# Performance work log

Measured on AMD Instinct MI355X. Metric: run time of the kernel, lower is better.

## Reference

```python
import jax, jax.numpy as jnp
import numpy as np

N, D = 262144, 512
EPS = 1e-6  # flax LayerNorm default


def setup_inputs() -> dict:
    key = jax.random.key(0)
    kx, kw = jax.random.split(key)
    x = jax.random.normal(kx, (N, D), dtype=jnp.float32)
    # LayerNorm params (flax defaults: scale init ones, bias init zeros)
    ln_scale = jnp.ones((D,), dtype=jnp.float32)
    ln_bias = jnp.zeros((D,), dtype=jnp.float32)
    # Dense params (lecun_normal kernel init approximated by scaled normal)
    kernel = jax.random.normal(kw, (D, D), dtype=jnp.float32) / jnp.sqrt(jnp.float32(D))
    bias = jnp.zeros((D,), dtype=jnp.float32)
    return {"x": x, "ln_scale": ln_scale, "ln_bias": ln_bias, "kernel": kernel, "bias": bias}


def reference(x, ln_scale, ln_bias, kernel, bias):
    # LayerNorm over last axis
    mu = jnp.mean(x, axis=-1, keepdims=True)
    var = jnp.mean(jnp.square(x - mu), axis=-1, keepdims=True)
    out = (x - mu) * jax.lax.rsqrt(var + EPS) * ln_scale + ln_bias
    # activation -> Dense -> residual add
    h = jax.nn.relu(out)
    return x + jnp.dot(h, kernel) + bias
```

## Files before the change

### kernel.cpp

```cpp
#include <hip/hip_runtime.h>
#include <hip/hip_bf16.h>

#define DD 512
#define BM 32
#define THREADS 512

typedef __attribute__((ext_vector_type(8))) short short8;
typedef __attribute__((ext_vector_type(4))) float f32x4;

__device__ __forceinline__ unsigned short f2bf(float f) {
  union { float f; unsigned u; } v; v.f = f;
  unsigned r = v.u + 0x7FFFu + ((v.u >> 16) & 1u);
  return (unsigned short)(r >> 16);
}
__device__ __forceinline__ float bf2f(unsigned short u) {
  union { unsigned u; float f; } v; v.u = ((unsigned)u) << 16;
  return v.f;
}

__global__ void prep_bpack(const float* __restrict__ W, unsigned short* __restrict__ Bpack) {
  const int tid = blockIdx.x * blockDim.x + threadIdx.x;
  const int n = tid & 511, k = tid >> 9;
  const float w = W[(size_t)k * DD + n];
  const int nb = n >> 4, lo = n & 15;
  const int kt = k >> 5, hi = (k >> 3) & 3, j = k & 7;
  const int lane = hi * 16 + lo;
  Bpack[(((size_t)(nb * 16 + kt)) * 64 + lane) * 8 + j] = f2bf(w);
}

__global__ __launch_bounds__(THREADS, 4)
void fused_ln_gemm(const float* __restrict__ x, const float* __restrict__ lns,
                   const float* __restrict__ lnb, const unsigned short* __restrict__ Bpack,
                   const float* __restrict__ bias, float* __restrict__ out) {
  __shared__ unsigned short Alds[BM * 512];
  __shared__ unsigned short Xlds[BM * 528];

  const int t = threadIdx.x;
  const long row0 = (long)blockIdx.x * BM;

  {
    const int r = t >> 4, g = t & 15;
    const float* xr = x + (row0 + r) * DD + g * 4;
    float4 v[8];
    float s = 0.f, s2 = 0.f;
    #pragma unroll
    for (int i = 0; i < 8; ++i) {
      v[i] = *(const float4*)(xr + i * 64);
      s  += (v[i].x + v[i].y) + (v[i].z + v[i].w);
      s2 += v[i].x * v[i].x + v[i].y * v[i].y + v[i].z * v[i].z + v[i].w * v[i].w;
    }
    #pragma unroll
    for (int m = 1; m < 16; m <<= 1) {
      s  += __shfl_xor(s,  m, 64);
      s2 += __shfl_xor(s2, m, 64);
    }
    const float mu   = s * (1.f / 512.f);
    const float var  = fmaxf(s2 * (1.f / 512.f) - mu * mu, 0.f);
    const float rstd = rsqrtf(var + 1e-6f);
    #pragma unroll
    for (int i = 0; i < 8; ++i) {
      const int c = g * 4 + i * 64;
      const float4 sc = *(const float4*)(lns + c);
      const float4 bi = *(const float4*)(lnb + c);
      float h0 = fmaxf((v[i].x - mu) * rstd * sc.x + bi.x, 0.f);
      float h1 = fmaxf((v[i].y - mu) * rstd * sc.y + bi.y, 0.f);
      float h2 = fmaxf((v[i].z - mu) * rstd * sc.z + bi.z, 0.f);
      float h3 = fmaxf((v[i].w - mu) * rstd * sc.w + bi.w, 0.f);
      ushort4 hu = { f2bf(h0), f2bf(h1), f2bf(h2), f2bf(h3) };
      ushort4 xu = { f2bf(v[i].x), f2bf(v[i].y), f2bf(v[i].z), f2bf(v[i].w) };
      unsigned a = (unsigned)(r * 1024 + g * 8 + i * 128) ^ (unsigned)((r & 7) << 4);
      *(ushort4*)((char*)Alds + a) = hu;
      *(ushort4*)(&Xlds[r * 528 + c]) = xu;
    }
  }
  __syncthreads();

  const int lane = t & 63, lo = lane & 15, hi = lane >> 4;
  const int wn = t >> 6;

  unsigned abase0, aswz0, abase1, aswz1;
  {
    const int r0 = lo;        abase0 = (unsigned)(r0 * 1024 + hi * 16); aswz0 = (unsigned)((r0 & 7) << 4);
    const int r1 = 16 + lo;   abase1 = (unsigned)(r1 * 1024 + hi * 16); aswz1 = (unsigned)((r1 & 7) << 4);
  }
  const short8* bbase = (const short8*)Bpack + (size_t)wn * 4096 + lane;

#define LOADB(dst, kt)                                                        \
  { dst##0 = bbase[(0 * 16 + (kt)) * 64];                                     \
    dst##1 = bbase[(1 * 16 + (kt)) * 64];                                     \
    dst##2 = bbase[(2 * 16 + (kt)) * 64];                                     \
    dst##3 = bbase[(3 * 16 + (kt)) * 64]; }

  short8 bA0, bA1, bA2, bA3, bB0, bB1, bB2, bB3, bC0, bC1, bC2, bC3;
  LOADB(bA, 0);
  LOADB(bB, 1);

  f32x4 acc00 = {}, acc01 = {}, acc02 = {}, acc03 = {};
  f32x4 acc10 = {}, acc11 = {}, acc12 = {}, acc13 = {};

  #pragma unroll
  for (int kt = 0; kt < 16; ++kt) {
    if (kt + 2 < 16) LOADB(bC, kt + 2);
    const short8 a0 = *(const short8*)((const char*)Alds + ((abase0 + (unsigned)kt * 64) ^ aswz0));
    const short8 a1 = *(const short8*)((const char*)Alds + ((abase1 + (unsigned)kt * 64) ^ aswz1));
    acc00 = __builtin_amdgcn_mfma_f32_16x16x32_bf16(a0, bA0, acc00, 0, 0, 0);
    acc10 = __builtin_amdgcn_mfma_f32_16x16x32_bf16(a1, bA0, acc10, 0, 0, 0);
    acc01 = __builtin_amdgcn_mfma_f32_16x16x32_bf16(a0, bA1, acc01, 0, 0, 0);
    acc11 = __builtin_amdgcn_mfma_f32_16x16x32_bf16(a1, bA1, acc11, 0, 0, 0);
    acc02 = __builtin_amdgcn_mfma_f32_16x16x32_bf16(a0, bA2, acc02, 0, 0, 0);
    acc12 = __builtin_amdgcn_mfma_f32_16x16x32_bf16(a1, bA2, acc12, 0, 0, 0);
    acc03 = __builtin_amdgcn_mfma_f32_16x16x32_bf16(a0, bA3, acc03, 0, 0, 0);
    acc13 = __builtin_amdgcn_mfma_f32_16x16x32_bf16(a1, bA3, acc13, 0, 0, 0);
    bA0 = bB0; bA1 = bB1; bA2 = bB2; bA3 = bB3;
    bB0 = bC0; bB1 = bC1; bB2 = bC2; bB3 = bC3;
  }
#undef LOADB

  f32x4 accs[2][4] = {{acc00, acc01, acc02, acc03}, {acc10, acc11, acc12, acc13}};
  #pragma unroll
  for (int m = 0; m < 2; ++m) {
    #pragma unroll
    for (int nt = 0; nt < 4; ++nt) {
      const int col = wn * 64 + nt * 16 + lo;
      const float bv = bias[col];
      #pragma unroll
      for (int q = 0; q < 4; ++q) {
        const int rloc = m * 16 + hi * 4 + q;
        const float xv = bf2f(Xlds[rloc * 528 + col]);
        out[(row0 + rloc) * DD + col] = xv + accs[m][nt][q] + bv;
      }
    }
  }
}

extern "C" void kernel_launch(void* const* d_in, const int* in_sizes, int n_in,
                              void* d_out, int out_size, void* d_ws, size_t ws_size,
                              hipStream_t stream) {
  const float* x    = (const float*)d_in[0];
  const float* lns  = (const float*)d_in[1];
  const float* lnb  = (const float*)d_in[2];
  const float* W    = (const float*)d_in[3];
  const float* bias = (const float*)d_in[4];
  float* out = (float*)d_out;
  unsigned short* Bpack = (unsigned short*)d_ws;

  const int nrows = in_sizes[0] / DD;

  prep_bpack<<<DD * DD / 256, 256, 0, stream>>>(W, Bpack);
  fused_ln_gemm<<<nrows / BM, THREADS, 0, stream>>>(x, lns, lnb, Bpack, bias, out);
}
```

Before: 336.7 us.

## Load x in MFMA output layout, keep residual in registers, drop Xlds buffer

Each thread now loads x elements at the positions its MFMA accumulators will write, keeping bf16-packed copies in registers for the residual instead of staging them in a 33KB LDS buffer. Row statistics are reduced via shuffles plus a small cross-wave LDS reduction, and the B-operand register prefetch pipeline is removed. Launch bounds are raised to 6 blocks per CU to exploit the lower LDS footprint. The trade-offs are strided 4-byte global loads instead of float4, scalar LDS stores for A, and loss of explicit B prefetching.

```diff
diff --git a/kernel.cpp b/kernel.cpp
--- a/kernel.cpp
+++ b/kernel.cpp
@@ -13,8 +13,8 @@
   unsigned r = v.u + 0x7FFFu + ((v.u >> 16) & 1u);
   return (unsigned short)(r >> 16);
 }
-__device__ __forceinline__ float bf2f(unsigned short u) {
-  union { unsigned u; float f; } v; v.u = ((unsigned)u) << 16;
+__device__ __forceinline__ float bf2f(unsigned u16) {
+  union { unsigned u; float f; } v; v.u = u16 << 16;
   return v.f;
 }
 
@@ -28,107 +28,144 @@
   Bpack[(((size_t)(nb * 16 + kt)) * 64 + lane) * 8 + j] = f2bf(w);
 }
 
-__global__ __launch_bounds__(THREADS, 4)
+__global__ __launch_bounds__(THREADS, 6)
 void fused_ln_gemm(const float* __restrict__ x, const float* __restrict__ lns,
                    const float* __restrict__ lnb, const unsigned short* __restrict__ Bpack,
                    const float* __restrict__ bias, float* __restrict__ out) {
   __shared__ unsigned short Alds[BM * 512];
-  __shared__ unsigned short Xlds[BM * 528];
+  __shared__ float s_lds[BM][8];
+  __shared__ float q_lds[BM][8];
 
   const int t = threadIdx.x;
+  const int lane = t & 63, lo = lane & 15, hi = lane >> 4;
+  const int wn = t >> 6;
   const long row0 = (long)blockIdx.x * BM;
 
+  float ps[8], pq[8];
+  unsigned xpk[16];
   {
-    const int r = t >> 4, g = t & 15;
-    const float* xr = x + (row0 + r) * DD + g * 4;
-    float4 v[8];
-    float s = 0.f, s2 = 0.f;
+    unsigned short tmp[4];
     #pragma unroll
-    for (int i = 0; i < 8; ++i) {
-      v[i] = *(const float4*)(xr + i * 64);
-      s  += (v[i].x + v[i].y) + (v[i].z + v[i].w);
-      s2 += v[i].x * v[i].x + v[i].y * v[i].y + v[i].z * v[i].z + v[i].w * v[i].w;
+    for (int m = 0; m < 2; ++m) {
+      #pragma unroll
+      for (int q = 0; q < 4; ++q) {
+        const float* xr = x + (row0 + m * 16 + hi * 4 + q) * DD + wn * 64 + lo;
+        const float v0 = xr[0], v1 = xr[16], v2 = xr[32], v3 = xr[48];
+        ps[m * 4 + q] = (v0 + v1) + (v2 + v3);
+        pq[m * 4 + q] = v0 * v0 + v1 * v1 + v2 * v2 + v3 * v3;
+        const unsigned short b0 = f2bf(v0), b1 = f2bf(v1), b2 = f2bf(v2), b3 = f2bf(v3);
+        if ((q & 1) == 0) {
+          tmp[0] = b0; tmp[1] = b1; tmp[2] = b2; tmp[3] = b3;
+        } else {
+          xpk[(m * 4 + 0) * 2 + (q >> 1)] = (unsigned)tmp[0] | ((unsigned)b0 << 16);
+          xpk[(m * 4 + 1) * 2 + (q >> 1)] = (unsigned)tmp[1] | ((unsigned)b1 << 16);
+          xpk[(m * 4 + 2) * 2 + (q >> 1)] = (unsigned)tmp[2] | ((unsigned)b2 << 16);
+          xpk[(m * 4 + 3) * 2 + (q >> 1)] = (unsigned)tmp[3] | ((unsigned)b3 << 16);
+        }
+      }
     }
+  }
+  #pragma unroll
+  for (int i = 0; i < 8; ++i) {
     #pragma unroll
-    for (int m = 1; m < 16; m <<= 1) {
-      s  += __shfl_xor(s,  m, 64);
-      s2 += __shfl_xor(s2, m, 64);
+    for (int msk = 1; msk < 16; msk <<= 1) {
+      ps[i] += __shfl_xor(ps[i], msk, 64);
+      pq[i] += __shfl_xor(pq[i], msk, 64);
     }
-    const float mu   = s * (1.f / 512.f);
-    const float var  = fmaxf(s2 * (1.f / 512.f) - mu * mu, 0.f);
-    const float rstd = rsqrtf(var + 1e-6f);
+  }
+  if (lo == 0) {
     #pragma unroll
-    for (int i = 0; i < 8; ++i) {
-      const int c = g * 4 + i * 64;
-      const float4 sc = *(const float4*)(lns + c);
-      const float4 bi = *(const float4*)(lnb + c);
-      float h0 = fmaxf((v[i].x - mu) * rstd * sc.x + bi.x, 0.f);
-      float h1 = fmaxf((v[i].y - mu) * rstd * sc.y + bi.y, 0.f);
-      float h2 = fmaxf((v[i].z - mu) * rstd * sc.z + bi.z, 0.f);
-      float h3 = fmaxf((v[i].w - mu) * rstd * sc.w + bi.w, 0.f);
-      ushort4 hu = { f2bf(h0), f2bf(h1), f2bf(h2), f2bf(h3) };
-      ushort4 xu = { f2bf(v[i].x), f2bf(v[i].y), f2bf(v[i].z), f2bf(v[i].w) };
-      unsigned a = (unsigned)(r * 1024 + g * 8 + i * 128) ^ (unsigned)((r & 7) << 4);
-      *(ushort4*)((char*)Alds + a) = hu;
-      *(ushort4*)(&Xlds[r * 528 + c]) = xu;
+    for (int m = 0; m < 2; ++m)
+      #pragma unroll
+      for (int q = 0; q < 4; ++q) {
+        const int r = m * 16 + hi * 4 + q;
+        s_lds[r][wn] = ps[m * 4 + q];
+        q_lds[r][wn] = pq[m * 4 + q];
+      }
+  }
+  __syncthreads();
+
+  {
+    float mu[8], rs[8];
+    #pragma unroll
+    for (int m = 0; m < 2; ++m)
+      #pragma unroll
+      for (int q = 0; q < 4; ++q) {
+        const int r = m * 16 + hi * 4 + q, i = m * 4 + q;
+        const float4 a = *(const float4*)&s_lds[r][0];
+        const float4 b = *(const float4*)&s_lds[r][4];
+        const float4 c = *(const float4*)&q_lds[r][0];
+        const float4 d = *(const float4*)&q_lds[r][4];
+        const float s  = ((a.x + a.y) + (a.z + a.w)) + ((b.x + b.y) + (b.z + b.w));
+        const float s2 = ((c.x + c.y) + (c.z + c.w)) + ((d.x + d.y) + (d.z + d.w));
+        mu[i] = s * (1.f / 512.f);
+        const float var = fmaxf(s2 * (1.f / 512.f) - mu[i] * mu[i], 0.f);
+        rs[i] = rsqrtf(var + 1e-6f);
+      }
+    #pragma unroll
+    for (int nt = 0; nt < 4; ++nt) {
+      const int col = wn * 64 + nt * 16 + lo;
+      const float sc = lns[col], bi = lnb[col];
+      #pragma unroll
+      for (int m = 0; m < 2; ++m)
+        #pragma unroll
+        for (int qq = 0; qq < 2; ++qq) {
+          const unsigned p = xpk[(m * 4 + nt) * 2 + qq];
+          const int i0 = m * 4 + qq * 2;
+          const unsigned short h0 = f2bf(fmaxf((bf2f(p & 0xffffu) - mu[i0]) * rs[i0] * sc + bi, 0.f));
+          const unsigned short h1 = f2bf(fmaxf((bf2f(p >> 16) - mu[i0 + 1]) * rs[i0 + 1] * sc + bi, 0.f));
+          const int r0 = m * 16 + hi * 4 + qq * 2;
+          const unsigned a0 = (unsigned)(r0 * 1024 + col * 2) ^ (unsigned)((r0 & 7) << 4);
+          const unsigned a1 = (unsigned)((r0 + 1) * 1024 + col * 2) ^ (unsigned)(((r0 + 1) & 7) << 4);
+          *(unsigned short*)((char*)Alds + a0) = h0;
+          *(unsigned short*)((char*)Alds + a1) = h1;
+        }
     }
   }
   __syncthreads();
 
-  const int lane = t & 63, lo = lane & 15, hi = lane >> 4;
-  const int wn = t >> 6;
-
   unsigned abase0, aswz0, abase1, aswz1;
   {
-    const int r0 = lo;        abase0 = (unsigned)(r0 * 1024 + hi * 16); aswz0 = (unsigned)((r0 & 7) << 4);
-    const int r1 = 16 + lo;   abase1 = (unsigned)(r1 * 1024 + hi * 16); aswz1 = (unsigned)((r1 & 7) << 4);
+    const int r0 = lo;       abase0 = (unsigned)(r0 * 1024 + hi * 16); aswz0 = (unsigned)((r0 & 7) << 4);
+    const int r1 = 16 + lo;  abase1 = (unsigned)(r1 * 1024 + hi * 16); aswz1 = (unsigned)((r1 & 7) << 4);
   }
   const short8* bbase = (const short8*)Bpack + (size_t)wn * 4096 + lane;
-
-#define LOADB(dst, kt)                                                        \
-  { dst##0 = bbase[(0 * 16 + (kt)) * 64];                                     \
-    dst##1 = bbase[(1 * 16 + (kt)) * 64];                                     \
-    dst##2 = bbase[(2 * 16 + (kt)) * 64];                                     \
-    dst##3 = bbase[(3 * 16 + (kt)) * 64]; }
-
-  short8 bA0, bA1, bA2, bA3, bB0, bB1, bB2, bB3, bC0, bC1, bC2, bC3;
-  LOADB(bA, 0);
-  LOADB(bB, 1);
 
   f32x4 acc00 = {}, acc01 = {}, acc02 = {}, acc03 = {};
   f32x4 acc10 = {}, acc11 = {}, acc12 = {}, acc13 = {};
 
   #pragma unroll
   for (int kt = 0; kt < 16; ++kt) {
-    if (kt + 2 < 16) LOADB(bC, kt + 2);
+    const short8 b0 = bbase[(0 * 16 + kt) * 64];
+    const short8 b1 = bbase[(1 * 16 + kt) * 64];
+    const short8 b2 = bbase[(2 * 16 + kt) * 64];
+    const short8 b3 = bbase[(3 * 16 + kt) * 64];
     const short8 a0 = *(const short8*)((const char*)Alds + ((abase0 + (unsigned)kt * 64) ^ aswz0));
     const short8 a1 = *(const short8*)((const char*)Alds + ((abase1 + (unsigned)kt * 64) ^ aswz1));
-    acc00 = __builtin_amdgcn_mfma_f32_16x16x32_bf16(a0, bA0, acc00, 0, 0, 0);
-    acc10 = __builtin_amdgcn_mfma_f32_16x16x32_bf16(a1, bA0, acc10, 0, 0, 0);
-    acc01 = __builtin_amdgcn_mfma_f32_16x16x32_bf16(a0, bA1, acc01, 0, 0, 0);
-    acc11 = __builtin_amdgcn_mfma_f32_16x16x32_bf16(a1, bA1, acc11, 0, 0, 0);
-    acc02 = __builtin_amdgcn_mfma_f32_16x16x32_bf16(a0, bA2, acc02, 0, 0, 0);
-    acc12 = __builtin_amdgcn_mfma_f32_16x16x32_bf16(a1, bA2, acc12, 0, 0, 0);
-    acc03 = __builtin_amdgcn_mfma_f32_16x16x32_bf16(a0, bA3, acc03, 0, 0, 0);
-    acc13 = __builtin_amdgcn_mfma_f32_16x16x32_bf16(a1, bA3, acc13, 0, 0, 0);
-    bA0 = bB0; bA1 = bB1; bA2 = bB2; bA3 = bB3;
-    bB0 = bC0; bB1 = bC1; bB2 = bC2; bB3 = bC3;
+    acc00 = __builtin_amdgcn_mfma_f32_16x16x32_bf16(a0, b0, acc00, 0, 0, 0);
+    acc10 = __builtin_amdgcn_mfma_f32_16x16x32_bf16(a1, b0, acc10, 0, 0, 0);
+    acc01 = __builtin_amdgcn_mfma_f32_16x16x32_bf16(a0, b1, acc01, 0, 0, 0);
+    acc11 = __builtin_amdgcn_mfma_f32_16x16x32_bf16(a1, b1, acc11, 0, 0, 0);
+    acc02 = __builtin_amdgcn_mfma_f32_16x16x32_bf16(a0, b2, acc02, 0, 0, 0);
+    acc12 = __builtin_amdgcn_mfma_f32_16x16x32_bf16(a1, b2, acc12, 0, 0, 0);
+    acc03 = __builtin_amdgcn_mfma_f32_16x16x32_bf16(a0, b3, acc03, 0, 0, 0);
+    acc13 = __builtin_amdgcn_mfma_f32_16x16x32_bf16(a1, b3, acc13, 0, 0, 0);
   }
-#undef LOADB
 
-  f32x4 accs[2][4] = {{acc00, acc01, acc02, acc03}, {acc10, acc11, acc12, acc13}};
-  #pragma unroll
-  for (int m = 0; m < 2; ++m) {
+  {
+    const f32x4 accs[2][4] = {{acc00, acc01, acc02, acc03}, {acc10, acc11, acc12, acc13}};
     #pragma unroll
     for (int nt = 0; nt < 4; ++nt) {
       const int col = wn * 64 + nt * 16 + lo;
       const float bv = bias[col];
       #pragma unroll
-      for (int q = 0; q < 4; ++q) {
-        const int rloc = m * 16 + hi * 4 + q;
-        const float xv = bf2f(Xlds[rloc * 528 + col]);
-        out[(row0 + rloc) * DD + col] = xv + accs[m][nt][q] + bv;
-      }
+      for (int m = 0; m < 2; ++m)
+        #pragma unroll
+        for (int q = 0; q < 4; ++q) {
+          const unsigned p = xpk[(m * 4 + nt) * 2 + (q >> 1)];
+          const float xv = bf2f((q & 1) ? (p >> 16) : (p & 0xffffu));
+          out[(row0 + m * 16 + hi * 4 + q) * DD + col] = accs[m][nt][q] + xv + bv;
+        }
     }
   }
 }
```

Result: slower. 759.1 us (+125.5%).

## Drop bf16 residual LDS copy, seed accumulators with x+bias, raise occupancy

Applied to the files above, without the earlier changes.

Removes the Xlds shared buffer that held a bf16 copy of x. Instead, the MFMA accumulators are initialised from a full-precision global re-read of x plus bias, so the epilogue only stores. It also drops the explicit three-deep B register prefetch and raises the launch-bounds occupancy hint from 4 to 6. Together these cut LDS use and register pressure so more blocks can be resident. The cost is a second global read of x (likely served from L2) and less explicit latency hiding on the B loads.

```diff
diff --git a/kernel.cpp b/kernel.cpp
--- a/kernel.cpp
+++ b/kernel.cpp
@@ -13,10 +13,6 @@
   unsigned r = v.u + 0x7FFFu + ((v.u >> 16) & 1u);
   return (unsigned short)(r >> 16);
 }
-__device__ __forceinline__ float bf2f(unsigned short u) {
-  union { unsigned u; float f; } v; v.u = ((unsigned)u) << 16;
-  return v.f;
-}
 
 __global__ void prep_bpack(const float* __restrict__ W, unsigned short* __restrict__ Bpack) {
   const int tid = blockIdx.x * blockDim.x + threadIdx.x;
@@ -28,12 +24,11 @@
   Bpack[(((size_t)(nb * 16 + kt)) * 64 + lane) * 8 + j] = f2bf(w);
 }
 
-__global__ __launch_bounds__(THREADS, 4)
+__global__ __launch_bounds__(THREADS, 6)
 void fused_ln_gemm(const float* __restrict__ x, const float* __restrict__ lns,
                    const float* __restrict__ lnb, const unsigned short* __restrict__ Bpack,
                    const float* __restrict__ bias, float* __restrict__ out) {
   __shared__ unsigned short Alds[BM * 512];
-  __shared__ unsigned short Xlds[BM * 528];
 
   const int t = threadIdx.x;
   const long row0 = (long)blockIdx.x * BM;
@@ -62,15 +57,13 @@
       const int c = g * 4 + i * 64;
       const float4 sc = *(const float4*)(lns + c);
       const float4 bi = *(const float4*)(lnb + c);
-      float h0 = fmaxf((v[i].x - mu) * rstd * sc.x + bi.x, 0.f);
-      float h1 = fmaxf((v[i].y - mu) * rstd * sc.y + bi.y, 0.f);
-      float h2 = fmaxf((v[i].z - mu) * rstd * sc.z + bi.z, 0.f);
-      float h3 = fmaxf((v[i].w - mu) * rstd * sc.w + bi.w, 0.f);
-      ushort4 hu = { f2bf(h0), f2bf(h1), f2bf(h2), f2bf(h3) };
-      ushort4 xu = { f2bf(v[i].x), f2bf(v[i].y), f2bf(v[i].z), f2bf(v[i].w) };
-      unsigned a = (unsigned)(r * 1024 + g * 8 + i * 128) ^ (unsigned)((r & 7) << 4);
+      ushort4 hu;
+      hu.x = f2bf(fmaxf((v[i].x - mu) * rstd * sc.x + bi.x, 0.f));
+      hu.y = f2bf(fmaxf((v[i].y - mu) * rstd * sc.y + bi.y, 0.f));
+      hu.z = f2bf(fmaxf((v[i].z - mu) * rstd * sc.z + bi.z, 0.f));
+      hu.w = f2bf(fmaxf((v[i].w - mu) * rstd * sc.w + bi.w, 0.f));
+      const unsigned a = (unsigned)(r * 1024 + g * 8 + i * 128) ^ (unsigned)((r & 7) << 4);
       *(ushort4*)((char*)Alds + a) = hu;
-      *(ushort4*)(&Xlds[r * 528 + c]) = xu;
     }
   }
   __syncthreads();
@@ -78,58 +71,55 @@
   const int lane = t & 63, lo = lane & 15, hi = lane >> 4;
   const int wn = t >> 6;
 
+  const float* xc = x + (row0 + hi * 4) * DD + wn * 64 + lo;
+  const float bv0 = bias[wn * 64 +  0 + lo];
+  const float bv1 = bias[wn * 64 + 16 + lo];
+  const float bv2 = bias[wn * 64 + 32 + lo];
+  const float bv3 = bias[wn * 64 + 48 + lo];
+
+  f32x4 acc00, acc01, acc02, acc03, acc10, acc11, acc12, acc13;
+  #pragma unroll
+  for (int q = 0; q < 4; ++q) {
+    const float* r0 = xc + q * DD;
+    const float* r1 = xc + (16 * DD) + q * DD;
+    acc00[q] = r0[ 0] + bv0;  acc01[q] = r0[16] + bv1;
+    acc02[q] = r0[32] + bv2;  acc03[q] = r0[48] + bv3;
+    acc10[q] = r1[ 0] + bv0;  acc11[q] = r1[16] + bv1;
+    acc12[q] = r1[32] + bv2;  acc13[q] = r1[48] + bv3;
+  }
+
   unsigned abase0, aswz0, abase1, aswz1;
   {
-    const int r0 = lo;        abase0 = (unsigned)(r0 * 1024 + hi * 16); aswz0 = (unsigned)((r0 & 7) << 4);
-    const int r1 = 16 + lo;   abase1 = (unsigned)(r1 * 1024 + hi * 16); aswz1 = (unsigned)((r1 & 7) << 4);
+    const int r0 = lo;       abase0 = (unsigned)(r0 * 1024 + hi * 16); aswz0 = (unsigned)((r0 & 7) << 4);
+    const int r1 = 16 + lo;  abase1 = (unsigned)(r1 * 1024 + hi * 16); aswz1 = (unsigned)((r1 & 7) << 4);
   }
   const short8* bbase = (const short8*)Bpack + (size_t)wn * 4096 + lane;
 
-#define LOADB(dst, kt)                                                        \
-  { dst##0 = bbase[(0 * 16 + (kt)) * 64];                                     \
-    dst##1 = bbase[(1 * 16 + (kt)) * 64];                                     \
-    dst##2 = bbase[(2 * 16 + (kt)) * 64];                                     \
-    dst##3 = bbase[(3 * 16 + (kt)) * 64]; }
-
-  short8 bA0, bA1, bA2, bA3, bB0, bB1, bB2, bB3, bC0, bC1, bC2, bC3;
-  LOADB(bA, 0);
-  LOADB(bB, 1);
-
-  f32x4 acc00 = {}, acc01 = {}, acc02 = {}, acc03 = {};
-  f32x4 acc10 = {}, acc11 = {}, acc12 = {}, acc13 = {};
-
   #pragma unroll
   for (int kt = 0; kt < 16; ++kt) {
-    if (kt + 2 < 16) LOADB(bC, kt + 2);
+    const short8 b0 = bbase[(0 * 16 + kt) * 64];
+    const short8 b1 = bbase[(1 * 16 + kt) * 64];
+    const short8 b2 = bbase[(2 * 16 + kt) * 64];
+    const short8 b3 = bbase[(3 * 16 + kt) * 64];
     const short8 a0 = *(const short8*)((const char*)Alds + ((abase0 + (unsigned)kt * 64) ^ aswz0));
     const short8 a1 = *(const short8*)((const char*)Alds + ((abase1 + (unsigned)kt * 64) ^ aswz1));
-    acc00 = __builtin_amdgcn_mfma_f32_16x16x32_bf16(a0, bA0, acc00, 0, 0, 0);
-    acc10 = __builtin_amdgcn_mfma_f32_16x16x32_bf16(a1, bA0, acc10, 0, 0, 0);
-    acc01 = __builtin_amdgcn_mfma_f32_16x16x32_bf16(a0, bA1, acc01, 0, 0, 0);
-    acc11 = __builtin_amdgcn_mfma_f32_16x16x32_bf16(a1, bA1, acc11, 0, 0, 0);
-    acc02 = __builtin_amdgcn_mfma_f32_16x16x32_bf16(a0, bA2, acc02, 0, 0, 0);
-    acc12 = __builtin_amdgcn_mfma_f32_16x16x32_bf16(a1, bA2, acc12, 0, 0, 0);
-    acc03 = __builtin_amdgcn_mfma_f32_16x16x32_bf16(a0, bA3, acc03, 0, 0, 0);
-    acc13 = __builtin_amdgcn_mfma_f32_16x16x32_bf16(a1, bA3, acc13, 0, 0, 0);
-    bA0 = bB0; bA1 = bB1; bA2 = bB2; bA3 = bB3;
-    bB0 = bC0; bB1 = bC1; bB2 = bC2; bB3 = bC3;
+    acc00 = __builtin_amdgcn_mfma_f32_16x16x32_bf16(a0, b0, acc00, 0, 0, 0);
+    acc10 = __builtin_amdgcn_mfma_f32_16x16x32_bf16(a1, b0, acc10, 0, 0, 0);
+    acc01 = __builtin_amdgcn_mfma_f32_16x16x32_bf16(a0, b1, acc01, 0, 0, 0);
+    acc11 = __builtin_amdgcn_mfma_f32_16x16x32_bf16(a1, b1, acc11, 0, 0, 0);
+    acc02 = __builtin_amdgcn_mfma_f32_16x16x32_bf16(a0, b2, acc02, 0, 0, 0);
+    acc12 = __builtin_amdgcn_mfma_f32_16x16x32_bf16(a1, b2, acc12, 0, 0, 0);
+    acc03 = __builtin_amdgcn_mfma_f32_16x16x32_bf16(a0, b3, acc03, 0, 0, 0);
+    acc13 = __builtin_amdgcn_mfma_f32_16x16x32_bf16(a1, b3, acc13, 0, 0, 0);
   }
-#undef LOADB
 
-  f32x4 accs[2][4] = {{acc00, acc01, acc02, acc03}, {acc10, acc11, acc12, acc13}};
+  float* oc = out + (row0 + hi * 4) * DD + wn * 64 + lo;
   #pragma unroll
-  for (int m = 0; m < 2; ++m) {
-    #pragma unroll
-    for (int nt = 0; nt < 4; ++nt) {
-      const int col = wn * 64 + nt * 16 + lo;
-      const float bv = bias[col];
-      #pragma unroll
-      for (int q = 0; q < 4; ++q) {
-        const int rloc = m * 16 + hi * 4 + q;
-        const float xv = bf2f(Xlds[rloc * 528 + col]);
-        out[(row0 + rloc) * DD + col] = xv + accs[m][nt][q] + bv;
-      }
-    }
+  for (int q = 0; q < 4; ++q) {
+    float* r0 = oc + q * DD;
+    float* r1 = oc + (16 * DD) + q * DD;
+    r0[ 0] = acc00[q];  r0[16] = acc01[q];  r0[32] = acc02[q];  r0[48] = acc03[q];
+    r1[ 0] = acc10[q];  r1[16] = acc11[q];  r1[32] = acc12[q];  r1[48] = acc13[q];
   }
 }
 
```

Measured after the change: 362.9 us. 7.8% more time.
